# Kernel optimization log

Measured on AMD Instinct MI355X. Metric: run time of the kernel, lower is better.

## Reference

```python
import jax, jax.numpy as jnp
import numpy as np

EMBED = 1024
HEADS = 16
HEAD_DIM = EMBED // HEADS


def setup_inputs() -> dict:
    key = jax.random.key(0)
    ks = jax.random.split(key, 11)
    N, S = 2, 2048
    scale = 1.0 / np.sqrt(EMBED)
    inp = {
        "values": jax.random.normal(ks[0], (N, S, EMBED), jnp.float32),
        "keys": jax.random.normal(ks[1], (N, S, EMBED), jnp.float32),
        "queries": jax.random.normal(ks[2], (N, S, EMBED), jnp.float32),
        "W_v": jax.random.normal(ks[3], (EMBED, EMBED), jnp.float32) * scale,
        "b_v": jnp.zeros((EMBED,), jnp.float32),
        "W_k": jax.random.normal(ks[4], (EMBED, EMBED), jnp.float32) * scale,
        "b_k": jnp.zeros((EMBED,), jnp.float32),
        "W_q": jax.random.normal(ks[5], (EMBED, EMBED), jnp.float32) * scale,
        "b_q": jnp.zeros((EMBED,), jnp.float32),
        "W_o": jax.random.normal(ks[6], (EMBED, EMBED), jnp.float32) * scale,
        "b_o": jnp.zeros((EMBED,), jnp.float32),
    }
    return inp


def reference(values, keys, queries, W_v, b_v, W_k, b_k, W_q, b_q, W_o, b_o):
    N, q_len, _ = queries.shape
    # linear projections then split heads: [N, S, H, Dh]
    v = (values @ W_v.T + b_v).reshape(N, -1, HEADS, HEAD_DIM)
    k = (keys @ W_k.T + b_k).reshape(N, -1, HEADS, HEAD_DIM)
    q = (queries @ W_q.T + b_q).reshape(N, q_len, HEADS, HEAD_DIM)
    # raw scores [N, H, Q, K]
    energy = jnp.einsum("nqhd,nkhd->nhqk", q, k)
    attention = jax.nn.softmax(energy / np.sqrt(HEAD_DIM), axis=-1)
    out = jnp.einsum("nhql,nlhd->nqhd", attention, v).reshape(N, q_len, EMBED)
    return out @ W_o.T + b_o
```

## Files before the change

kernel.cpp:

```cpp
#include <hip/hip_runtime.h>
#include <hip/hip_bf16.h>


typedef short bf16x8 __attribute__((ext_vector_type(8)));
typedef short bf16x4 __attribute__((ext_vector_type(4)));
typedef float f32x4 __attribute__((ext_vector_type(4)));
typedef float f32x16 __attribute__((ext_vector_type(16)));
typedef unsigned u32x2 __attribute__((ext_vector_type(2)));
typedef unsigned u32x4 __attribute__((ext_vector_type(4)));

constexpr int S = 2048;
constexpr int E = 1024;
constexpr int H = 16;
constexpr int D = 64;
constexpr int M = 2 * S;
#define QSCALE 0.18033688011112042f

static __device__ __forceinline__ short f2bf_rne(float x) {
  unsigned u = __builtin_bit_cast(unsigned, x);
  u += 0x7fff + ((u >> 16) & 1);
  return (short)(u >> 16);
}
static __device__ __forceinline__ bf16x8 cvt8(float4 a, float4 b) {
  bf16x8 t;
  t[0] = f2bf_rne(a.x); t[1] = f2bf_rne(a.y);
  t[2] = f2bf_rne(a.z); t[3] = f2bf_rne(a.w);
  t[4] = f2bf_rne(b.x); t[5] = f2bf_rne(b.y);
  t[6] = f2bf_rne(b.z); t[7] = f2bf_rne(b.w);
  return t;
}
static __device__ __forceinline__ float fast_exp2(float x) {
#if __has_builtin(__builtin_amdgcn_exp2f)
  return __builtin_amdgcn_exp2f(x);
#else
  return __expf(0.69314718055994531f * x);
#endif
}
static __device__ __forceinline__ unsigned cvtpk(float a, float b) {
  unsigned r;
  asm("v_cvt_pk_bf16_f32 %0, %1, %2" : "=v"(r) : "v"(a), "v"(b));
  return r;
}
static __device__ __forceinline__ void plswap(unsigned& a, unsigned& b) {
#if __has_builtin(__builtin_amdgcn_permlane32_swap)
  u32x2 t = __builtin_amdgcn_permlane32_swap(a, b, false, false);
  a = t[0]; b = t[1];
#else
  asm("v_permlane32_swap_b32 %0, %1" : "+v"(a), "+v"(b));
#endif
}

static __device__ __forceinline__ void gl_lds16(const short* g, short* l) {
  __builtin_amdgcn_global_load_lds(
      (const __attribute__((address_space(1))) void*)g,
      (__attribute__((address_space(3))) void*)l, 16, 0, 0);
}


__global__ __launch_bounds__(256) void cast_a(
    const float* __restrict__ qs, const float* __restrict__ ks,
    const float* __restrict__ wq, const float* __restrict__ wk,
    const float* __restrict__ wv, const float* __restrict__ wo,
    short* __restrict__ qbf, short* __restrict__ kbf, short* __restrict__ wqb,
    short* __restrict__ wkb, short* __restrict__ wvb, short* __restrict__ wob) {
  const float* s;
  short* d;
  switch (blockIdx.y) {
    case 0: s = qs; d = qbf; break;
    case 1: s = ks; d = kbf; break;
    case 2: if (blockIdx.x >= 512) return; s = wq; d = wqb; break;
    case 3: if (blockIdx.x >= 512) return; s = wk; d = wkb; break;
    case 4: if (blockIdx.x >= 512) return; s = wv; d = wvb; break;
    default: if (blockIdx.x >= 512) return; s = wo; d = wob; break;
  }
  size_t i = ((size_t)blockIdx.x * 256 + threadIdx.x) * 8;
  *(bf16x8*)&d[i] = cvt8(*(const float4*)&s[i], *(const float4*)&s[i + 4]);
}

__global__ __launch_bounds__(256) void cast_one(const float* __restrict__ s,
                                                short* __restrict__ d) {
  size_t i = ((size_t)blockIdx.x * 256 + threadIdx.x) * 8;
  *(bf16x8*)&d[i] = cvt8(*(const float4*)&s[i], *(const float4*)&s[i + 4]);
}

__global__ __launch_bounds__(256) void qk_gemm(
    const short* __restrict__ qbf, const short* __restrict__ kbf,
    const short* __restrict__ wqb, const short* __restrict__ wkb,
    const float* __restrict__ bq, const float* __restrict__ bk,
    short* __restrict__ qb, short* __restrict__ kb) {
  __shared__ __align__(16) short as[128 * 32];
  __shared__ __align__(16) short bs[128 * 32];
  const int tid = threadIdx.x;
  const int lane = tid & 63, w = tid >> 6;
  const int l15 = lane & 15, quad = lane >> 4;
  const int wm = w & 1, wn = w >> 1;

  const int b = blockIdx.x;
  const int c = b & 7, r = b >> 3;
  const int bn = r & 7;
  const int t = c * 8 + (r >> 3);
  const int z = t >> 5, bm = t & 31;

  const short* A = z ? kbf : qbf;
  const short* Bw = z ? wkb : wqb;
  const float* bias = z ? bk : bq;

  const short* agp[2];
  const short* bgp[2];
  int ldsb[2];
#pragma unroll
  for (int cc = 0; cc < 2; ++cc) {
    int seg = w * 2 + cc;
    int p = seg * 8 + (lane >> 3), kc = lane & 7;
    int l = kc ^ (p & 7);
    int row = 2 * p + (l >> 2), col = (l & 3) * 8;
    ldsb[cc] = seg * 512;
    agp[cc] = &A[(size_t)(bm * 128 + row) * E + col];
    bgp[cc] = &Bw[(size_t)(bn * 128 + row) * E + col];
  }

  f32x4 acc[4][4] = {};
  for (int k0 = 0; k0 < E; k0 += 32) {
    __syncthreads();
#pragma unroll
    for (int cc = 0; cc < 2; ++cc) {
      gl_lds16(agp[cc] + k0, &as[ldsb[cc]]);
      gl_lds16(bgp[cc] + k0, &bs[ldsb[cc]]);
    }
    __syncthreads();

    bf16x8 af[4], bf[4];
#pragma unroll
    for (int tt = 0; tt < 4; ++tt) {
      int ra = wm * 64 + tt * 16 + l15;
      int pa2 = ra >> 1, la = (ra & 1) * 4 + quad, ka = la ^ (pa2 & 7);
      af[tt] = *(bf16x8*)&as[pa2 * 64 + ka * 8];
      int rb = wn * 64 + tt * 16 + l15;
      int pb2 = rb >> 1, lb = (rb & 1) * 4 + quad, kb2 = lb ^ (pb2 & 7);
      bf[tt] = *(bf16x8*)&bs[pb2 * 64 + kb2 * 8];
    }
#pragma unroll
    for (int mt = 0; mt < 4; ++mt)
#pragma unroll
      for (int nt = 0; nt < 4; ++nt)
        acc[mt][nt] = __builtin_amdgcn_mfma_f32_16x16x32_bf16(
            af[mt], bf[nt], acc[mt][nt], 0, 0, 0);
  }

#pragma unroll
  for (int mt = 0; mt < 4; ++mt)
#pragma unroll
    for (int nt = 0; nt < 4; ++nt)
#pragma unroll
      for (int rr = 0; rr < 4; ++rr) {
        int row = bm * 128 + wm * 64 + mt * 16 + quad * 4 + rr;
        int col = bn * 128 + wn * 64 + nt * 16 + l15;
        float v = acc[mt][nt][rr] + bias[col];
        int n = row >> 11, s = row & 2047, h = col >> 6, d = col & 63;
        if (z == 0) {
          qb[(((size_t)(n * H + h) * S) + s) * D + d] = f2bf_rne(v * QSCALE);
        } else {
          kb[(((size_t)(n * H + h) * S) + s) * D + d] = f2bf_rne(v);
        }
      }
}

template <int MODE>
__global__ __launch_bounds__(256) void gemm64(const short* __restrict__ A,
                                              const short* __restrict__ Bw,
                                              const float* __restrict__ bias,
                                              void* __restrict__ outp) {
  __shared__ __align__(16) short as[64 * 32];
  __shared__ __align__(16) short bs[128 * 32];
  const int tid = threadIdx.x;
  const int lane = tid & 63, w = tid >> 6;
  const int l15 = lane & 15, quad = lane >> 4;
  const int wm = w & 1, wn = w >> 1;

  const int b = blockIdx.x;
  const int c = b & 7, r = b >> 3;
  const int bn = r & 7;
  const int bm = c * 8 + (r >> 3);

  const short* agp;
  int aldsb;
  {
    int seg = w;
    int p = seg * 8 + (lane >> 3), kc = lane & 7;
    int l = kc ^ (p & 7);
    int row = 2 * p + (l >> 2), col = (l & 3) * 8;
    aldsb = seg * 512;
    agp = &A[(size_t)(bm * 64 + row) * E + col];
  }
  const short* bgp[2];
  int bldsb[2];
#pragma unroll
  for (int cc = 0; cc < 2; ++cc) {
    int seg = w * 2 + cc;
    int p = seg * 8 + (lane >> 3), kc = lane & 7;
    int l = kc ^ (p & 7);
    int row = 2 * p + (l >> 2), col = (l & 3) * 8;
    bldsb[cc] = seg * 512;
    bgp[cc] = &Bw[(size_t)(bn * 128 + row) * E + col];
  }

  f32x4 acc[2][4] = {};
  for (int k0 = 0; k0 < E; k0 += 32) {
    __syncthreads();
    gl_lds16(agp + k0, &as[aldsb]);
#pragma unroll
    for (int cc = 0; cc < 2; ++cc) gl_lds16(bgp[cc] + k0, &bs[bldsb[cc]]);
    __syncthreads();

    bf16x8 af[2], bf[4];
#pragma unroll
    for (int tt = 0; tt < 2; ++tt) {
      int ra = wm * 32 + tt * 16 + l15;
      int pa2 = ra >> 1, la = (ra & 1) * 4 + quad, ka = la ^ (pa2 & 7);
      af[tt] = *(bf16x8*)&as[pa2 * 64 + ka * 8];
    }
#pragma unroll
    for (int tt = 0; tt < 4; ++tt) {
      int rb = wn * 64 + tt * 16 + l15;
      int pb2 = rb >> 1, lb = (rb & 1) * 4 + quad, kb2 = lb ^ (pb2 & 7);
      bf[tt] = *(bf16x8*)&bs[pb2 * 64 + kb2 * 8];
    }
#pragma unroll
    for (int mt = 0; mt < 2; ++mt)
#pragma unroll
      for (int nt = 0; nt < 4; ++nt)
        acc[mt][nt] = __builtin_amdgcn_mfma_f32_16x16x32_bf16(
            af[mt], bf[nt], acc[mt][nt], 0, 0, 0);
  }

#pragma unroll
  for (int mt = 0; mt < 2; ++mt)
#pragma unroll
    for (int nt = 0; nt < 4; ++nt)
#pragma unroll
      for (int rr = 0; rr < 4; ++rr) {
        int row = bm * 64 + wm * 32 + mt * 16 + quad * 4 + rr;
        int col = bn * 128 + wn * 64 + nt * 16 + l15;
        float v = acc[mt][nt][rr] + bias[col];
        if (MODE == 0) {
          int n = row >> 11, s = row & 2047, h = col >> 6, d = col & 63;
          ((short*)outp)[(((size_t)(n * H + h) * D) + d) * S + s] =
              f2bf_rne(v);
        } else {
          ((float*)outp)[(size_t)row * E + col] = v;
        }
      }
}

__global__ __launch_bounds__(512) void attn_kernel(const short* __restrict__ q,
                                                   const short* __restrict__ k,
                                                   const short* __restrict__ vt,
                                                   short* __restrict__ ctx) {
  __shared__ __align__(16) short ks[128 * 72];
  __shared__ __align__(16) short vs[64 * 136];

  const int tid = threadIdx.x;
  const int lane = tid & 63, wv = tid >> 6;
  const int l31 = lane & 31, h = lane >> 5;

  const int bid = blockIdx.y * gridDim.x + blockIdx.x;
  const int c = bid & 7, r = bid >> 3;
  const int qt = r & 7;
  const int hz = c * 4 + (r >> 3);
  const int hh = hz & 15, nn = hz >> 4;

  const size_t base = (size_t)(nn * H + hh) * S * D;
  const int q0 = qt * 256 + wv * 32;

  bf16x8 qf[4];
#pragma unroll
  for (int kd = 0; kd < 4; ++kd)
    qf[kd] = *(const bf16x8*)&q[base + (size_t)(q0 + l31) * D + kd * 16 + h * 8];

  f32x16 o[2] = {};
  float lsum = 0.f;

  bf16x8 pk[2], pv[2];
  auto loadKV = [&](int j0) {
#pragma unroll
    for (int cc = 0; cc < 2; ++cc) {
      int ch = cc * 512 + tid;
      int kr = ch >> 3, kc = (ch & 7) * 8;
      pk[cc] = *(const bf16x8*)&k[base + (size_t)(j0 + kr) * D + kc];
      int vr = ch >> 4, vc = (ch & 15) * 8;
      pv[cc] = *(const bf16x8*)&vt[base + (size_t)vr * S + j0 + vc];
    }
  };

  loadKV(0);
  for (int j0 = 0; j0 < S; j0 += 128) {
    __syncthreads();
#pragma unroll
    for (int cc = 0; cc < 2; ++cc) {
      int ch = cc * 512 + tid;
      int kr = ch >> 3, kc = (ch & 7) * 8;
      *(bf16x8*)&ks[kr * 72 + kc] = pk[cc];
      int vr = ch >> 4, vc = (ch & 15) * 8;
      *(bf16x8*)&vs[vr * 136 + vc] = pv[cc];
    }
    __syncthreads();
    if (j0 + 128 < S) loadKV(j0 + 128);

#pragma unroll
    for (int half = 0; half < 2; ++half) {
      f32x16 sc[2] = {};
#pragma unroll
      for (int c2 = 0; c2 < 2; ++c2)
#pragma unroll
        for (int kd = 0; kd < 4; ++kd) {
          bf16x8 kf = *(bf16x8*)&ks[(half * 64 + c2 * 32 + l31) * 72 +
                                    kd * 16 + h * 8];
          sc[c2] = __builtin_amdgcn_mfma_f32_32x32x16_bf16(kf, qf[kd], sc[c2],
                                                           0, 0, 0);
        }

      bf16x8 pa[4];
#pragma unroll
      for (int c2 = 0; c2 < 2; ++c2) {
        float pe[16];
#pragma unroll
        for (int rr = 0; rr < 16; ++rr) {
          float p = fast_exp2(sc[c2][rr]);
          lsum += p;
          pe[rr] = p;
        }
#pragma unroll
        for (int kk = 0; kk < 2; ++kk) {
          unsigned A0 = cvtpk(pe[8 * kk + 0], pe[8 * kk + 1]);
          unsigned A1 = cvtpk(pe[8 * kk + 2], pe[8 * kk + 3]);
          unsigned B0 = cvtpk(pe[8 * kk + 4], pe[8 * kk + 5]);
          unsigned B1 = cvtpk(pe[8 * kk + 6], pe[8 * kk + 7]);
          plswap(A0, B0);
          plswap(A1, B1);
          u32x4 t;
          t[0] = A0; t[1] = A1; t[2] = B0; t[3] = B1;
          pa[c2 * 2 + kk] = __builtin_bit_cast(bf16x8, t);
        }
      }

#pragma unroll
      for (int ks2 = 0; ks2 < 4; ++ks2)
#pragma unroll
        for (int dc = 0; dc < 2; ++dc) {
          bf16x8 vf = *(bf16x8*)&vs[(dc * 32 + l31) * 136 + half * 64 +
                                    ks2 * 16 + h * 8];
          o[dc] = __builtin_amdgcn_mfma_f32_32x32x16_bf16(pa[ks2], vf, o[dc],
                                                          0, 0, 0);
        }
    }
  }

  lsum += __shfl_xor(lsum, 32);
  float invq = 1.0f / lsum;

#pragma unroll
  for (int rr = 0; rr < 16; ++rr) {
    int crow = (rr & 3) + 8 * (rr >> 2) + 4 * h;
    float inv = __shfl(invq, crow);
    int row = q0 + crow;
#pragma unroll
    for (int dc = 0; dc < 2; ++dc) {
      ctx[((size_t)(nn * S + row)) * E + hh * D + dc * 32 + l31] =
          f2bf_rne(o[dc][rr] * inv);
    }
  }
}

extern "C" void kernel_launch(void* const* d_in, const int* in_sizes, int n_in,
                              void* d_out, int out_size, void* d_ws,
                              size_t ws_size, hipStream_t stream) {
  const float* values  = (const float*)d_in[0];
  const float* keys    = (const float*)d_in[1];
  const float* queries = (const float*)d_in[2];
  const float* b_v = (const float*)d_in[4];
  const float* b_k = (const float*)d_in[6];
  const float* b_q = (const float*)d_in[8];
  const float* W_v = (const float*)d_in[3];
  const float* W_k = (const float*)d_in[5];
  const float* W_q = (const float*)d_in[7];
  const float* W_o = (const float*)d_in[9];
  const float* b_o = (const float*)d_in[10];

  const size_t X = (size_t)M * E;
  const size_t W = (size_t)E * E;

  short* qb  = (short*)d_out;
  short* qbf = (short*)d_out + X;
  short* kb      = (short*)d_ws;
  short* vtb     = kb + X;
  short* castbuf = vtb + X;
  short* wqb = castbuf + X;
  short* wkb = wqb + W;
  short* wvb = wkb + W;
  short* wob = wvb + W;
  short* kbf = castbuf;
  short* vbf = castbuf;
  short* ctx = castbuf;

  cast_a<<<dim3(2048, 6), 256, 0, stream>>>(queries, keys, W_q, W_k, W_v, W_o,
                                            qbf, kbf, wqb, wkb, wvb, wob);
  qk_gemm<<<512, 256, 0, stream>>>(qbf, kbf, wqb, wkb, b_q, b_k, qb, kb);
  cast_one<<<2048, 256, 0, stream>>>(values, vbf);
  gemm64<0><<<512, 256, 0, stream>>>(vbf, wvb, b_v, vtb);
  attn_kernel<<<dim3(8, 32), 512, 0, stream>>>(qb, kb, vtb, ctx);
  gemm64<1><<<512, 256, 0, stream>>>(ctx, wob, b_o, d_out);
}
```

Measured before the change: 217.9 us.

## Split attention keys across wave halves and fuse value cast into cast kernel

The attention kernel now gives each block 128 queries instead of 256 and splits every 128-key tile between two groups of four waves. Each group accumulates a partial output and row sum, and the two are merged through shared memory at the end. This doubles the grid to 512 blocks, so each CU can hold more resident waves, at the cost of reloading K/V tiles per block and an extra LDS reduction. Separately, the value-to-bf16 cast is folded into the main cast kernel, dropping one launch. Workspace buffers are reassigned and the V projection is launched before the Q/K projection so aliased buffers stay valid.

New measurement: 220.2 us. About the same (+1.1%).

```diff
diff --git a/kernel.cpp b/kernel.cpp
--- a/kernel.cpp
+++ b/kernel.cpp
@@ -57,28 +57,24 @@
 }
 
 
-__global__ __launch_bounds__(256) void cast_a(
+__global__ __launch_bounds__(256) void cast_all(
     const float* __restrict__ qs, const float* __restrict__ ks,
-    const float* __restrict__ wq, const float* __restrict__ wk,
-    const float* __restrict__ wv, const float* __restrict__ wo,
-    short* __restrict__ qbf, short* __restrict__ kbf, short* __restrict__ wqb,
+    const float* __restrict__ vsrc, const float* __restrict__ wq,
+    const float* __restrict__ wk, const float* __restrict__ wv,
+    const float* __restrict__ wo, short* __restrict__ qbf,
+    short* __restrict__ kbf, short* __restrict__ vbf, short* __restrict__ wqb,
     short* __restrict__ wkb, short* __restrict__ wvb, short* __restrict__ wob) {
   const float* s;
   short* d;
   switch (blockIdx.y) {
     case 0: s = qs; d = qbf; break;
     case 1: s = ks; d = kbf; break;
-    case 2: if (blockIdx.x >= 512) return; s = wq; d = wqb; break;
-    case 3: if (blockIdx.x >= 512) return; s = wk; d = wkb; break;
-    case 4: if (blockIdx.x >= 512) return; s = wv; d = wvb; break;
+    case 2: s = vsrc; d = vbf; break;
+    case 3: if (blockIdx.x >= 512) return; s = wq; d = wqb; break;
+    case 4: if (blockIdx.x >= 512) return; s = wk; d = wkb; break;
+    case 5: if (blockIdx.x >= 512) return; s = wv; d = wvb; break;
     default: if (blockIdx.x >= 512) return; s = wo; d = wob; break;
   }
-  size_t i = ((size_t)blockIdx.x * 256 + threadIdx.x) * 8;
-  *(bf16x8*)&d[i] = cvt8(*(const float4*)&s[i], *(const float4*)&s[i + 4]);
-}
-
-__global__ __launch_bounds__(256) void cast_one(const float* __restrict__ s,
-                                                short* __restrict__ d) {
   size_t i = ((size_t)blockIdx.x * 256 + threadIdx.x) * 8;
   *(bf16x8*)&d[i] = cvt8(*(const float4*)&s[i], *(const float4*)&s[i + 4]);
 }
@@ -256,21 +252,24 @@
                                                    const short* __restrict__ k,
                                                    const short* __restrict__ vt,
                                                    short* __restrict__ ctx) {
-  __shared__ __align__(16) short ks[128 * 72];
-  __shared__ __align__(16) short vs[64 * 136];
+  __shared__ __align__(16) short smem[128 * 72 + 64 * 136];
+  short* ks = smem;
+  short* vs = smem + 128 * 72;
+  float* mrg = (float*)smem;
 
   const int tid = threadIdx.x;
   const int lane = tid & 63, wv = tid >> 6;
   const int l31 = lane & 31, h = lane >> 5;
+  const int qg = wv & 3, kh = wv >> 2;
 
   const int bid = blockIdx.y * gridDim.x + blockIdx.x;
   const int c = bid & 7, r = bid >> 3;
-  const int qt = r & 7;
-  const int hz = c * 4 + (r >> 3);
+  const int qt = r & 15;
+  const int hz = c * 4 + (r >> 4);
   const int hh = hz & 15, nn = hz >> 4;
 
   const size_t base = (size_t)(nn * H + hh) * S * D;
-  const int q0 = qt * 256 + wv * 32;
+  const int q0 = qt * 128 + qg * 32;
 
   bf16x8 qf[4];
 #pragma unroll
@@ -306,67 +305,80 @@
     __syncthreads();
     if (j0 + 128 < S) loadKV(j0 + 128);
 
-#pragma unroll
-    for (int half = 0; half < 2; ++half) {
-      f32x16 sc[2] = {};
-#pragma unroll
-      for (int c2 = 0; c2 < 2; ++c2)
-#pragma unroll
-        for (int kd = 0; kd < 4; ++kd) {
-          bf16x8 kf = *(bf16x8*)&ks[(half * 64 + c2 * 32 + l31) * 72 +
-                                    kd * 16 + h * 8];
-          sc[c2] = __builtin_amdgcn_mfma_f32_32x32x16_bf16(kf, qf[kd], sc[c2],
-                                                           0, 0, 0);
-        }
-
-      bf16x8 pa[4];
-#pragma unroll
-      for (int c2 = 0; c2 < 2; ++c2) {
-        float pe[16];
-#pragma unroll
-        for (int rr = 0; rr < 16; ++rr) {
-          float p = fast_exp2(sc[c2][rr]);
-          lsum += p;
-          pe[rr] = p;
-        }
-#pragma unroll
-        for (int kk = 0; kk < 2; ++kk) {
-          unsigned A0 = cvtpk(pe[8 * kk + 0], pe[8 * kk + 1]);
-          unsigned A1 = cvtpk(pe[8 * kk + 2], pe[8 * kk + 3]);
-          unsigned B0 = cvtpk(pe[8 * kk + 4], pe[8 * kk + 5]);
-          unsigned B1 = cvtpk(pe[8 * kk + 6], pe[8 * kk + 7]);
-          plswap(A0, B0);
-          plswap(A1, B1);
-          u32x4 t;
-          t[0] = A0; t[1] = A1; t[2] = B0; t[3] = B1;
-          pa[c2 * 2 + kk] = __builtin_bit_cast(bf16x8, t);
-        }
-      }
-
-#pragma unroll
-      for (int ks2 = 0; ks2 < 4; ++ks2)
-#pragma unroll
-        for (int dc = 0; dc < 2; ++dc) {
-          bf16x8 vf = *(bf16x8*)&vs[(dc * 32 + l31) * 136 + half * 64 +
-                                    ks2 * 16 + h * 8];
-          o[dc] = __builtin_amdgcn_mfma_f32_32x32x16_bf16(pa[ks2], vf, o[dc],
-                                                          0, 0, 0);
-        }
-    }
+    f32x16 sc[2] = {};
+#pragma unroll
+    for (int c2 = 0; c2 < 2; ++c2)
+#pragma unroll
+      for (int kd = 0; kd < 4; ++kd) {
+        bf16x8 kf = *(bf16x8*)&ks[(kh * 64 + c2 * 32 + l31) * 72 +
+                                  kd * 16 + h * 8];
+        sc[c2] = __builtin_amdgcn_mfma_f32_32x32x16_bf16(kf, qf[kd], sc[c2],
+                                                         0, 0, 0);
+      }
+
+    bf16x8 pa[4];
+#pragma unroll
+    for (int c2 = 0; c2 < 2; ++c2) {
+      float pe[16];
+#pragma unroll
+      for (int rr = 0; rr < 16; ++rr) {
+        float p = fast_exp2(sc[c2][rr]);
+        lsum += p;
+        pe[rr] = p;
+      }
+#pragma unroll
+      for (int kk = 0; kk < 2; ++kk) {
+        unsigned A0 = cvtpk(pe[8 * kk + 0], pe[8 * kk + 1]);
+        unsigned A1 = cvtpk(pe[8 * kk + 2], pe[8 * kk + 3]);
+        unsigned B0 = cvtpk(pe[8 * kk + 4], pe[8 * kk + 5]);
+        unsigned B1 = cvtpk(pe[8 * kk + 6], pe[8 * kk + 7]);
+        plswap(A0, B0);
+        plswap(A1, B1);
+        u32x4 t;
+        t[0] = A0; t[1] = A1; t[2] = B0; t[3] = B1;
+        pa[c2 * 2 + kk] = __builtin_bit_cast(bf16x8, t);
+      }
+    }
+
+#pragma unroll
+    for (int ks2 = 0; ks2 < 4; ++ks2)
+#pragma unroll
+      for (int dc = 0; dc < 2; ++dc) {
+        bf16x8 vf = *(bf16x8*)&vs[(dc * 32 + l31) * 136 + kh * 64 +
+                                  ks2 * 16 + h * 8];
+        o[dc] = __builtin_amdgcn_mfma_f32_32x32x16_bf16(pa[ks2], vf, o[dc],
+                                                        0, 0, 0);
+      }
   }
 
   lsum += __shfl_xor(lsum, 32);
-  float invq = 1.0f / lsum;
-
-#pragma unroll
-  for (int rr = 0; rr < 16; ++rr) {
-    int crow = (rr & 3) + 8 * (rr >> 2) + 4 * h;
-    float inv = __shfl(invq, crow);
-    int row = q0 + crow;
-#pragma unroll
-    for (int dc = 0; dc < 2; ++dc) {
-      ctx[((size_t)(nn * S + row)) * E + hh * D + dc * 32 + l31] =
-          f2bf_rne(o[dc][rr] * inv);
+
+  __syncthreads();
+  if (kh == 1) {
+#pragma unroll
+    for (int rr = 0; rr < 16; ++rr) {
+      int crow = (rr & 3) + 8 * (rr >> 2) + 4 * h;
+#pragma unroll
+      for (int dc = 0; dc < 2; ++dc)
+        mrg[qg * 2080 + crow * 64 + dc * 32 + l31] = o[dc][rr];
+    }
+    if (h == 0) mrg[qg * 2080 + 2048 + l31] = lsum;
+  }
+  __syncthreads();
+  if (kh == 0) {
+    lsum += mrg[qg * 2080 + 2048 + l31];
+    float invq = 1.0f / lsum;
+#pragma unroll
+    for (int rr = 0; rr < 16; ++rr) {
+      int crow = (rr & 3) + 8 * (rr >> 2) + 4 * h;
+      float inv = __shfl(invq, crow);
+      int row = q0 + crow;
+#pragma unroll
+      for (int dc = 0; dc < 2; ++dc) {
+        float val = o[dc][rr] + mrg[qg * 2080 + crow * 64 + dc * 32 + l31];
+        ctx[((size_t)(nn * S + row)) * E + hh * D + dc * 32 + l31] =
+            f2bf_rne(val * inv);
+      }
     }
   }
 }
@@ -389,24 +401,23 @@
   const size_t X = (size_t)M * E;
   const size_t W = (size_t)E * E;
 
-  short* qb  = (short*)d_out;
-  short* qbf = (short*)d_out + X;
-  short* kb      = (short*)d_ws;
-  short* vtb     = kb + X;
-  short* castbuf = vtb + X;
-  short* wqb = castbuf + X;
+  short* qbf = (short*)d_out;
+  short* qb  = (short*)d_out + X;
+  short* kbf = (short*)d_ws;
+  short* vbf = kbf + X;
+  short* vtb = vbf + X;
+  short* wqb = vtb + X;
   short* wkb = wqb + W;
   short* wvb = wkb + W;
   short* wob = wvb + W;
-  short* kbf = castbuf;
-  short* vbf = castbuf;
-  short* ctx = castbuf;
-
-  cast_a<<<dim3(2048, 6), 256, 0, stream>>>(queries, keys, W_q, W_k, W_v, W_o,
-                                            qbf, kbf, wqb, wkb, wvb, wob);
+  short* ctx = kbf;
+  short* kb  = vbf;
+
+  cast_all<<<dim3(2048, 7), 256, 0, stream>>>(queries, keys, values, W_q, W_k,
+                                              W_v, W_o, qbf, kbf, vbf, wqb,
+                                              wkb, wvb, wob);
+  gemm64<0><<<512, 256, 0, stream>>>(vbf, wvb, b_v, vtb);
   qk_gemm<<<512, 256, 0, stream>>>(qbf, kbf, wqb, wkb, b_q, b_k, qb, kb);
-  cast_one<<<2048, 256, 0, stream>>>(values, vbf);
-  gemm64<0><<<512, 256, 0, stream>>>(vbf, wvb, b_v, vtb);
-  attn_kernel<<<dim3(8, 32), 512, 0, stream>>>(qb, kb, vtb, ctx);
+  attn_kernel<<<dim3(16, 32), 512, 0, stream>>>(qb, kb, vtb, ctx);
   gemm64<1><<<512, 256, 0, stream>>>(ctx, wob, b_o, d_out);
 }
```
